# Kernel optimization log

Measured on AMD Instinct MI355X. Metric: run time of the kernel, lower is better.

## Reference

```python
import jax, jax.numpy as jnp
import numpy as np

B, T, D = 1, 2048, 1024
E, DFF = 8, 4096


def setup_inputs() -> dict:
    key = jax.random.key(0)
    k1, k2, k3, k4 = jax.random.split(key, 4)
    x = jax.random.normal(k1, (B, T, D), dtype=jnp.float32)
    Wg = jax.random.normal(k2, (D, E), dtype=jnp.float32) * (1.0 / np.sqrt(D))
    w1 = jax.random.normal(k3, (D, DFF), dtype=jnp.float32) * (1.0 / np.sqrt(D))
    w2 = jax.random.normal(k4, (DFF, D), dtype=jnp.float32) * (1.0 / np.sqrt(DFF))
    return {"x": x, "Wg": Wg, "w1": w1, "w2": w2}


def _gating(logits):
    # logits: [S, E]; capacity = S (per source code)
    S, num_e = logits.shape
    gates = jax.nn.softmax(logits.astype(jnp.float32), axis=1)  # [S,E] fp32
    idx1 = jnp.argmax(gates, axis=1)                            # top-1 expert
    mask1 = jax.nn.one_hot(idx1, num_e, dtype=jnp.int32)        # [S,E]
    logits_ex1 = jnp.where(mask1.astype(bool), -jnp.inf, logits)
    idx2 = jnp.argmax(logits_ex1, axis=1)                       # top-2 expert
    mask2 = jax.nn.one_hot(idx2, num_e, dtype=jnp.int32)
    # slot position of each token inside its expert buffer
    loc1 = jnp.cumsum(mask1, axis=0) - 1                        # [S,E]
    loc2 = jnp.cumsum(mask2, axis=0) - 1 + jnp.sum(mask1, axis=0, keepdims=True)
    loc1_s = jnp.sum(loc1 * mask1, axis=1)                      # [S] int
    loc2_s = jnp.sum(loc2 * mask2, axis=1)
    g1 = jnp.sum(gates * mask1, axis=1)                         # [S]
    g2 = jnp.sum(gates * mask2, axis=1)
    denom = jnp.maximum(g1 + g2, jnp.finfo(jnp.float32).eps)
    g1, g2 = g1 / denom, g2 / denom
    cap = S
    loc1_sc = jax.nn.one_hot(loc1_s, cap, dtype=jnp.float32)    # [S,C]
    loc2_sc = jax.nn.one_hot(loc2_s, cap, dtype=jnp.float32)
    # combine_weights: [S,E,C]
    combine = (g1[:, None] * mask1)[:, :, None] * loc1_sc[:, None, :] \
            + (g2[:, None] * mask2)[:, :, None] * loc2_sc[:, None, :]
    dispatch_mask = combine != 0
    return combine.astype(logits.dtype), dispatch_mask


def reference(x, Wg, w1, w2):
    d_model = x.shape[2]
    xs = x.reshape(-1, d_model)                                  # [S,D]
    logits = xs @ Wg                                             # gate linear
    combine, dispatch_mask = _gating(logits)
    # one-hot scatter dispatch: [S,E,C] x [S,D] -> [E,C,D]
    dispatched = jnp.einsum('sec,sm->ecm', dispatch_mask.astype(jnp.float32), xs)
    # all-to-all is an identity permutation of the expert dim in single-process ref
    expert_out = jax.nn.relu(dispatched @ w1) @ w2               # [E,C,D]
    # one-hot gather combine: [S,E,C] x [E,C,D] -> [S,D]
    out = jnp.einsum('sec,ecm->sm', combine, expert_out)
    return out.reshape(x.shape)
```

## Files before the change

kernel.cpp:

```cpp
#include <hip/hip_runtime.h>
#include <stdint.h>


typedef __attribute__((ext_vector_type(4))) float f32x4;
typedef __attribute__((ext_vector_type(16))) float f32x16;
typedef __attribute__((ext_vector_type(8))) short bf16x8;

#define GPTR(p) (const __attribute__((address_space(1))) void*)(p)
#define LPTR(p) (__attribute__((address_space(3))) void*)(p)

__device__ __forceinline__ ushort f2bf(float f) {
  uint32_t u = __float_as_uint(f);
  uint32_t r = (u + 0x7FFFu + ((u >> 16) & 1u)) >> 16;
  return (ushort)r;
}
__device__ __forceinline__ float bf2f(ushort u) {
  return __uint_as_float((uint32_t)u << 16);
}

__global__ __launch_bounds__(256) void prep(const float* __restrict__ x,
                                            const float* __restrict__ w1,
                                            const float* __restrict__ w2,
                                            ushort* __restrict__ xb,
                                            ushort* __restrict__ w1t,
                                            ushort* __restrict__ w2t) {
  const int b = blockIdx.x, tid = threadIdx.x;
  if (b < 2048) {
    int i = b * 256 + tid;
    float4 v = ((const float4*)x)[i];
    ushort4 o;
    o.x = f2bf(v.x); o.y = f2bf(v.y); o.z = f2bf(v.z); o.w = f2bf(v.w);
    ((ushort4*)xb)[i] = o;
    return;
  }
  const float* in;
  ushort* outp;
  int R, C, bt;
  if (b < 3072) { bt = b - 2048; in = w1; outp = w1t; R = 1024; C = 4096; }
  else          { bt = b - 3072; in = w2; outp = w2t; R = 4096; C = 1024; }
  const int ntx = C / 64;
  const int bx = bt % ntx, by = bt / ntx;
  const int c0 = bx * 64, r0 = by * 64;
  __shared__ float tile[64][65];
  const int tx = tid & 15, ty = tid >> 4;
#pragma unroll
  for (int rr = 0; rr < 64; rr += 16) {
    float4 v = *(const float4*)&in[(size_t)(r0 + ty + rr) * C + c0 + tx * 4];
    tile[ty + rr][tx * 4 + 0] = v.x;
    tile[ty + rr][tx * 4 + 1] = v.y;
    tile[ty + rr][tx * 4 + 2] = v.z;
    tile[ty + rr][tx * 4 + 3] = v.w;
  }
  __syncthreads();
#pragma unroll
  for (int cc = 0; cc < 64; cc += 16) {
    const int c = ty + cc;
    const int r = tx * 4;
    ushort4 o;
    o.x = f2bf(tile[r + 0][c]);
    o.y = f2bf(tile[r + 1][c]);
    o.z = f2bf(tile[r + 2][c]);
    o.w = f2bf(tile[r + 3][c]);
    *(ushort4*)&outp[(size_t)(c0 + c) * R + r0 + r] = o;
  }
}

__global__ void reduce_out(float* __restrict__ out, const ushort* __restrict__ pb,
                           int SD) {
  int i = blockIdx.x * blockDim.x + threadIdx.x;
  if (i >= SD / 4) return;
  f32x4 a = ((const f32x4*)out)[i];
#pragma unroll
  for (int j = 0; j < 3; ++j) {
    ushort4 u = ((const ushort4*)(pb + (size_t)j * SD))[i];
    a[0] += bf2f(u.x); a[1] += bf2f(u.y); a[2] += bf2f(u.z); a[3] += bf2f(u.w);
  }
  ((f32x4*)out)[i] = a;
}

template <int MODE>
__global__ __launch_bounds__(512) void gemm_pipe(const ushort* __restrict__ A,
                                                 const ushort* __restrict__ Bt,
                                                 void* __restrict__ C0,
                                                 void* __restrict__ C1,
                                                 int M, int N, int Ks, int Ktot,
                                                 int ncx, int cpz) {
  constexpr int BM = 128, BN = 256, BK = 64;
  __shared__ ushort As[3][BM * BK];
  __shared__ ushort Bs[3][BN * BK];

  const int tid = threadIdx.x;
  const int lane = tid & 63, wid = tid >> 6;
  const int wr = wid >> 2, wc = wid & 3;

  const int ck = blockIdx.x & 7;
  const int w = blockIdx.x >> 3;
  const int bz = ck / cpz;
  const int rem = ck % cpz;
  const int bx = (rem % ncx) * 4 + (w & 3);
  const int by = (rem / ncx) * 8 + (w >> 2);
  const int row0 = by * BM, col0 = bx * BN;
  const int kbase = bz * Ks;

  f32x16 acc[2][2];
#pragma unroll
  for (int m = 0; m < 2; ++m)
#pragma unroll
    for (int n = 0; n < 2; ++n) acc[m][n] = (f32x16)(0.f);

  const int rA = tid >> 3;
  const int cb = (tid & 7) * 16;
  auto stage_part = [&](int buf, int k0, int p) {
    if (p == 0) {
#pragma unroll
      for (int i = 0; i < 2; ++i) {
        int r = i * 64 + rA;
        int csw = cb ^ ((r & 7) << 4);
        __builtin_amdgcn_global_load_lds(
            GPTR((const char*)(A + (size_t)(row0 + r) * Ktot + k0) + csw),
            LPTR((char*)&As[buf][0] + i * 8192 + wid * 1024), 16, 0, 0);
      }
    } else {
#pragma unroll
      for (int j2 = 0; j2 < 2; ++j2) {
        int j = (p - 1) * 2 + j2;
        int r = j * 64 + rA;
        int csw = cb ^ ((r & 7) << 4);
        __builtin_amdgcn_global_load_lds(
            GPTR((const char*)(Bt + (size_t)(col0 + r) * Ktot + k0) + csw),
            LPTR((char*)&Bs[buf][0] + j * 8192 + wid * 1024), 16, 0, 0);
      }
    }
  };

  const int nt = Ks / BK;
  stage_part(0, kbase, 0); stage_part(0, kbase, 1); stage_part(0, kbase, 2);
  stage_part(1, kbase + BK, 0); stage_part(1, kbase + BK, 1); stage_part(1, kbase + BK, 2);
  asm volatile("s_waitcnt vmcnt(6)" ::: "memory");
  __builtin_amdgcn_sched_barrier(0);
  __builtin_amdgcn_s_barrier();
  __builtin_amdgcn_sched_barrier(0);

  for (int t = 0; t < nt; ++t) {
    const ushort* Ab = As[t % 3];
    const ushort* Bb = Bs[t % 3];
    const bool pf = (t + 2 < nt);
    const int knext = kbase + (t + 2) * BK;
    const int pbuf = (t + 2) % 3;

#pragma unroll
    for (int p = 0; p < 2; ++p) {
      bf16x8 a2[2][2], b2[2][2];
#pragma unroll
      for (int sl = 0; sl < 2; ++sl) {
        const int s = p * 2 + sl;
        const int kb2 = s * 32 + (lane >> 5) * 16;
#pragma unroll
        for (int m = 0; m < 2; ++m) {
          int R = wr * 64 + m * 32 + (lane & 31);
          a2[sl][m] = *(const bf16x8*)((const char*)Ab + R * 128 + (kb2 ^ ((R & 7) << 4)));
        }
#pragma unroll
        for (int n = 0; n < 2; ++n) {
          int R = wc * 64 + n * 32 + (lane & 31);
          b2[sl][n] = *(const bf16x8*)((const char*)Bb + R * 128 + (kb2 ^ ((R & 7) << 4)));
        }
      }
      if (pf) {
        if (p == 0) { stage_part(pbuf, knext, 0); stage_part(pbuf, knext, 1); }
        else        { stage_part(pbuf, knext, 2); }
      }
      __builtin_amdgcn_sched_barrier(0);
      __builtin_amdgcn_s_barrier();
      asm volatile("s_waitcnt lgkmcnt(0)" ::: "memory");
      __builtin_amdgcn_sched_barrier(0);
      __builtin_amdgcn_s_setprio(1);
#pragma unroll
      for (int sl = 0; sl < 2; ++sl)
#pragma unroll
        for (int m = 0; m < 2; ++m)
#pragma unroll
          for (int n = 0; n < 2; ++n)
            acc[m][n] = __builtin_amdgcn_mfma_f32_32x32x16_bf16(a2[sl][m], b2[sl][n],
                                                                acc[m][n], 0, 0, 0);
      __builtin_amdgcn_s_setprio(0);
      __builtin_amdgcn_sched_barrier(0);
      if (p == 1 && t < nt - 1) {
        if (t + 2 < nt) asm volatile("s_waitcnt vmcnt(6)" ::: "memory");
        else            asm volatile("s_waitcnt vmcnt(0)" ::: "memory");
        __builtin_amdgcn_sched_barrier(0);
      }
      __builtin_amdgcn_s_barrier();
      __builtin_amdgcn_sched_barrier(0);
    }
  }

  const int rbase = row0 + wr * 64, cbase = col0 + wc * 64;
#pragma unroll
  for (int m = 0; m < 2; ++m) {
#pragma unroll
    for (int n = 0; n < 2; ++n) {
      const int col = cbase + n * 32 + (lane & 31);
#pragma unroll
      for (int r = 0; r < 16; ++r) {
        const int row = rbase + m * 32 + (r & 3) + 8 * (r >> 2) + 4 * (lane >> 5);
        float v = acc[m][n][r];
        size_t idx = (size_t)row * N + col;
        if (MODE == 1) {
          v = v > 0.f ? v : 0.f;
          ((ushort*)C0)[idx] = f2bf(v);
        } else {
          if (bz == 0)
            ((float*)C0)[idx] = v;
          else
            ((ushort*)C1)[(size_t)(bz - 1) * M * N + idx] = f2bf(v);
        }
      }
    }
  }
}

extern "C" void kernel_launch(void* const* d_in, const int* in_sizes, int n_in,
                              void* d_out, int out_size, void* d_ws, size_t ws_size,
                              hipStream_t stream) {
  const float* x  = (const float*)d_in[0];
  const float* w1 = (const float*)d_in[2];
  const float* w2 = (const float*)d_in[3];
  float* out = (float*)d_out;

  constexpr int S = 2048, D = 1024, F = 4096;
  char* ws = (char*)d_ws;
  ushort* xb  = (ushort*)(ws);
  ushort* w1t = (ushort*)(ws + (size_t)S * D * 2);
  ushort* w2t = (ushort*)(ws + (size_t)(S * D + F * D) * 2);
  ushort* H   = (ushort*)(ws + (size_t)(S * D + 2 * F * D) * 2);
  ushort* pb = (ushort*)(ws);

  hipLaunchKernelGGL(prep, dim3(4096), dim3(256), 0, stream,
                     x, w1, w2, xb, w1t, w2t);
  hipLaunchKernelGGL((gemm_pipe<1>), dim3(256), dim3(512), 0, stream,
                     xb, w1t, (void*)H, nullptr, S, F, D, D, 4, 8);
  hipLaunchKernelGGL((gemm_pipe<2>), dim3(256), dim3(512), 0, stream,
                     H, w2t, (void*)out, (void*)pb, S, D, F / 4, F, 1, 2);
  hipLaunchKernelGGL(reduce_out, dim3((S * D / 4 + 255) / 256), dim3(256), 0, stream,
                     out, pb, S * D);
}
```

Measured before the change: 70.68 us.

## Restructure GEMM k-loop to one barrier per tile with register double-buffered LDS reads

The GEMM main loop now synchronises once per k-tile instead of several times. It splits the tile into four k-slices, loading the next slice's LDS fragments into a second register buffer while the current slice's MFMAs run. The global-to-LDS prefetch for tile t+2 is spread across the slices. Separately, the prep, reduce and epilogue loads and stores use nontemporal hints to reduce cache pollution. The change trades extra register pressure and compiler-dependent scheduling (the explicit sched barriers are gone) for fewer barrier stalls.

```diff
diff --git a/kernel.cpp b/kernel.cpp
--- a/kernel.cpp
+++ b/kernel.cpp
@@ -5,6 +5,7 @@
 typedef __attribute__((ext_vector_type(4))) float f32x4;
 typedef __attribute__((ext_vector_type(16))) float f32x16;
 typedef __attribute__((ext_vector_type(8))) short bf16x8;
+typedef __attribute__((ext_vector_type(4))) ushort u16x4;
 
 #define GPTR(p) (const __attribute__((address_space(1))) void*)(p)
 #define LPTR(p) (__attribute__((address_space(3))) void*)(p)
@@ -27,10 +28,10 @@
   const int b = blockIdx.x, tid = threadIdx.x;
   if (b < 2048) {
     int i = b * 256 + tid;
-    float4 v = ((const float4*)x)[i];
-    ushort4 o;
+    f32x4 v = __builtin_nontemporal_load(&((const f32x4*)x)[i]);
+    u16x4 o;
     o.x = f2bf(v.x); o.y = f2bf(v.y); o.z = f2bf(v.z); o.w = f2bf(v.w);
-    ((ushort4*)xb)[i] = o;
+    ((u16x4*)xb)[i] = o;
     return;
   }
   const float* in;
@@ -45,7 +46,8 @@
   const int tx = tid & 15, ty = tid >> 4;
 #pragma unroll
   for (int rr = 0; rr < 64; rr += 16) {
-    float4 v = *(const float4*)&in[(size_t)(r0 + ty + rr) * C + c0 + tx * 4];
+    f32x4 v = __builtin_nontemporal_load(
+        (const f32x4*)&in[(size_t)(r0 + ty + rr) * C + c0 + tx * 4]);
     tile[ty + rr][tx * 4 + 0] = v.x;
     tile[ty + rr][tx * 4 + 1] = v.y;
     tile[ty + rr][tx * 4 + 2] = v.z;
@@ -56,12 +58,12 @@
   for (int cc = 0; cc < 64; cc += 16) {
     const int c = ty + cc;
     const int r = tx * 4;
-    ushort4 o;
+    u16x4 o;
     o.x = f2bf(tile[r + 0][c]);
     o.y = f2bf(tile[r + 1][c]);
     o.z = f2bf(tile[r + 2][c]);
     o.w = f2bf(tile[r + 3][c]);
-    *(ushort4*)&outp[(size_t)(c0 + c) * R + r0 + r] = o;
+    *(u16x4*)&outp[(size_t)(c0 + c) * R + r0 + r] = o;
   }
 }
 
@@ -69,13 +71,13 @@
                            int SD) {
   int i = blockIdx.x * blockDim.x + threadIdx.x;
   if (i >= SD / 4) return;
-  f32x4 a = ((const f32x4*)out)[i];
+  f32x4 a = __builtin_nontemporal_load(&((const f32x4*)out)[i]);
 #pragma unroll
   for (int j = 0; j < 3; ++j) {
-    ushort4 u = ((const ushort4*)(pb + (size_t)j * SD))[i];
+    u16x4 u = __builtin_nontemporal_load(&((const u16x4*)(pb + (size_t)j * SD))[i]);
     a[0] += bf2f(u.x); a[1] += bf2f(u.y); a[2] += bf2f(u.z); a[3] += bf2f(u.w);
   }
-  ((f32x4*)out)[i] = a;
+  __builtin_nontemporal_store(a, &((f32x4*)out)[i]);
 }
 
 template <int MODE>
@@ -132,66 +134,55 @@
       }
     }
   };
+  auto stage = [&](int buf, int k0) {
+    stage_part(buf, k0, 0); stage_part(buf, k0, 1); stage_part(buf, k0, 2);
+  };
 
   const int nt = Ks / BK;
-  stage_part(0, kbase, 0); stage_part(0, kbase, 1); stage_part(0, kbase, 2);
-  stage_part(1, kbase + BK, 0); stage_part(1, kbase + BK, 1); stage_part(1, kbase + BK, 2);
-  asm volatile("s_waitcnt vmcnt(6)" ::: "memory");
-  __builtin_amdgcn_sched_barrier(0);
-  __builtin_amdgcn_s_barrier();
-  __builtin_amdgcn_sched_barrier(0);
+  stage(0, kbase);
+  stage(1, kbase + BK);
 
   for (int t = 0; t < nt; ++t) {
+    if (t < nt - 1) asm volatile("s_waitcnt vmcnt(6)" ::: "memory");
+    else            asm volatile("s_waitcnt vmcnt(0)" ::: "memory");
+    __builtin_amdgcn_sched_barrier(0);
+    __builtin_amdgcn_s_barrier();
+    __builtin_amdgcn_sched_barrier(0);
+
     const ushort* Ab = As[t % 3];
     const ushort* Bb = Bs[t % 3];
     const bool pf = (t + 2 < nt);
     const int knext = kbase + (t + 2) * BK;
     const int pbuf = (t + 2) % 3;
 
-#pragma unroll
-    for (int p = 0; p < 2; ++p) {
-      bf16x8 a2[2][2], b2[2][2];
-#pragma unroll
-      for (int sl = 0; sl < 2; ++sl) {
-        const int s = p * 2 + sl;
-        const int kb2 = s * 32 + (lane >> 5) * 16;
-#pragma unroll
-        for (int m = 0; m < 2; ++m) {
-          int R = wr * 64 + m * 32 + (lane & 31);
-          a2[sl][m] = *(const bf16x8*)((const char*)Ab + R * 128 + (kb2 ^ ((R & 7) << 4)));
-        }
-#pragma unroll
-        for (int n = 0; n < 2; ++n) {
-          int R = wc * 64 + n * 32 + (lane & 31);
-          b2[sl][n] = *(const bf16x8*)((const char*)Bb + R * 128 + (kb2 ^ ((R & 7) << 4)));
-        }
-      }
-      if (pf) {
-        if (p == 0) { stage_part(pbuf, knext, 0); stage_part(pbuf, knext, 1); }
-        else        { stage_part(pbuf, knext, 2); }
-      }
-      __builtin_amdgcn_sched_barrier(0);
-      __builtin_amdgcn_s_barrier();
-      asm volatile("s_waitcnt lgkmcnt(0)" ::: "memory");
-      __builtin_amdgcn_sched_barrier(0);
+    bf16x8 a[2][2], b[2][2];
+    auto read_slice = [&](int s, int sb) {
+      const int kb2 = s * 32 + (lane >> 5) * 16;
+#pragma unroll
+      for (int m = 0; m < 2; ++m) {
+        int R = wr * 64 + m * 32 + (lane & 31);
+        a[sb][m] = *(const bf16x8*)((const char*)Ab + R * 128 + (kb2 ^ ((R & 7) << 4)));
+      }
+#pragma unroll
+      for (int n = 0; n < 2; ++n) {
+        int R = wc * 64 + n * 32 + (lane & 31);
+        b[sb][n] = *(const bf16x8*)((const char*)Bb + R * 128 + (kb2 ^ ((R & 7) << 4)));
+      }
+    };
+
+    read_slice(0, 0);
+#pragma unroll
+    for (int s = 0; s < 4; ++s) {
+      if (s < 3) read_slice(s + 1, (s + 1) & 1);
+      if (s < 3 && pf) stage_part(pbuf, knext, s);
       __builtin_amdgcn_s_setprio(1);
 #pragma unroll
-      for (int sl = 0; sl < 2; ++sl)
-#pragma unroll
-        for (int m = 0; m < 2; ++m)
-#pragma unroll
-          for (int n = 0; n < 2; ++n)
-            acc[m][n] = __builtin_amdgcn_mfma_f32_32x32x16_bf16(a2[sl][m], b2[sl][n],
-                                                                acc[m][n], 0, 0, 0);
+      for (int m = 0; m < 2; ++m)
+#pragma unroll
+        for (int n = 0; n < 2; ++n)
+          acc[m][n] = __builtin_amdgcn_mfma_f32_32x32x16_bf16(a[s & 1][m], b[s & 1][n],
+                                                              acc[m][n], 0, 0, 0);
       __builtin_amdgcn_s_setprio(0);
-      __builtin_amdgcn_sched_barrier(0);
-      if (p == 1 && t < nt - 1) {
-        if (t + 2 < nt) asm volatile("s_waitcnt vmcnt(6)" ::: "memory");
-        else            asm volatile("s_waitcnt vmcnt(0)" ::: "memory");
-        __builtin_amdgcn_sched_barrier(0);
-      }
-      __builtin_amdgcn_s_barrier();
-      __builtin_amdgcn_sched_barrier(0);
     }
   }
 
@@ -208,12 +199,13 @@
         size_t idx = (size_t)row * N + col;
         if (MODE == 1) {
           v = v > 0.f ? v : 0.f;
-          ((ushort*)C0)[idx] = f2bf(v);
+          __builtin_nontemporal_store(f2bf(v), &((ushort*)C0)[idx]);
         } else {
           if (bz == 0)
-            ((float*)C0)[idx] = v;
+            __builtin_nontemporal_store(v, &((float*)C0)[idx]);
           else
-            ((ushort*)C1)[(size_t)(bz - 1) * M * N + idx] = f2bf(v);
+            __builtin_nontemporal_store(f2bf(v),
+                &((ushort*)C1)[(size_t)(bz - 1) * M * N + idx]);
         }
       }
     }
```

Result: slower. 77.26 us (+9.3%).
